# Optimization experiments

Measured on AMD Instinct MI355X. Metric: run time of the kernel, lower is better.

## Reference

```python
import jax, jax.numpy as jnp
import numpy as np
from jax import lax

V, D, L = 32000, 1024, 8
HQ, HKV, HD = 16, 4, 64          # head_dim = D // HQ
H = int(2.6875 * D)              # SwiGLU hidden = 2752
B, S = 2, 1024
WINDOW, GEVERY = 256, 4
EPS, BASE = 1e-6, 10000.0
STD = 0.02


def setup_inputs() -> dict:
    key = jax.random.key(0)
    ks = jax.random.split(key, 10)
    return {
        "idx": jax.random.randint(ks[0], (B, S), 0, V, dtype=jnp.int32),
        "emb": jax.random.normal(ks[1], (V, D), jnp.float32) * STD,
        "Wq": jax.random.normal(ks[2], (L, D, HQ * HD), jnp.float32) * STD,
        "Wk": jax.random.normal(ks[3], (L, D, HKV * HD), jnp.float32) * STD,
        "Wv": jax.random.normal(ks[4], (L, D, HKV * HD), jnp.float32) * STD,
        "Wo": jax.random.normal(ks[5], (L, HQ * HD, D), jnp.float32) * (STD / np.sqrt(2 * L)).astype(np.float32),
        "w1": jax.random.normal(ks[6], (L, D, H), jnp.float32) * STD,
        "w3": jax.random.normal(ks[7], (L, D, H), jnp.float32) * STD,
        "w2": jax.random.normal(ks[8], (L, H, D), jnp.float32) * (STD / np.sqrt(2 * L)).astype(np.float32),
        "n1": jnp.ones((L, D), jnp.float32),
        "n2": jnp.ones((L, D), jnp.float32),
        "nf": jnp.ones((D,), jnp.float32),
    }


def _rmsnorm(x, w):
    return x * lax.rsqrt(jnp.mean(x * x, axis=-1, keepdims=True) + EPS) * w


def _rope(x, cos, sin):
    # x: [B,S,h,HD]; pairs (even, odd) rotated by complex multiply with e^{i*theta}
    x2 = x.reshape(*x.shape[:-1], HD // 2, 2)
    x0, x1 = x2[..., 0], x2[..., 1]
    r0 = x0 * cos - x1 * sin
    r1 = x0 * sin + x1 * cos
    return jnp.stack([r0, r1], axis=-1).reshape(x.shape)


def _forward(idx, emb, Wq, Wk, Wv, Wo, w1, w3, w2, n1, n2, nf):
    # RoPE cache (RoPECache._build_cache)
    inv_freq = 1.0 / (BASE ** (jnp.arange(0, HD, 2, dtype=jnp.float32) / HD))
    t = jnp.arange(S, dtype=jnp.float32)
    freqs = t[:, None] * inv_freq[None, :]                      # [S, HD//2]
    cos = jnp.cos(freqs)[None, :, None, :]                      # [1,S,1,HD//2]
    sin = jnp.sin(freqs)[None, :, None, :]

    # masks: global causal and sliding-window causal (additive, 0 / -inf)
    pos = jnp.arange(S)
    causal = pos[None, :] <= pos[:, None]
    local = causal & ((pos[:, None] - pos[None, :]) < WINDOW)
    neg_inf = jnp.float32(-jnp.inf)
    gmask = jnp.where(causal, 0.0, neg_inf).astype(jnp.float32)
    lmask = jnp.where(local, 0.0, neg_inf).astype(jnp.float32)
    use_global = ((jnp.arange(L) + 1) % GEVERY) == 0            # [L] bool

    scale = 1.0 / (HD ** 0.5)
    rep = HQ // HKV

    def block(x, p):
        wq, wk, wv, wo, W1, W3, W2, g1, g2, ug = p
        h = _rmsnorm(x, g1)
        q = (h @ wq).reshape(B, S, HQ, HD)
        k = (h @ wk).reshape(B, S, HKV, HD)
        v = (h @ wv).reshape(B, S, HKV, HD)
        q = _rope(q, cos, sin)
        k = _rope(k, cos, sin)
        k = jnp.repeat(k, rep, axis=2)                          # GQA: expand KV heads
        v = jnp.repeat(v, rep, axis=2)
        mask = jnp.where(ug, gmask, lmask)
        sc = jnp.einsum('bqhd,bkhd->bhqk', q, k) * scale + mask
        attn = jax.nn.softmax(sc, axis=-1)
        o = jnp.einsum('bhqk,bkhd->bqhd', attn, v).reshape(B, S, HQ * HD)
        x = x + o @ wo
        h2 = _rmsnorm(x, g2)
        x = x + (jax.nn.silu(h2 @ W1) * (h2 @ W3)) @ W2
        return x, None

    x = emb[idx]                                                # token embedding
    x, _ = lax.scan(block, x, (Wq, Wk, Wv, Wo, w1, w3, w2, n1, n2, use_global))
    logits = _rmsnorm(x, nf) @ emb.T                            # tied lm_head
    return logits


def reference(idx, emb, Wq, Wk, Wv, Wo, w1, w3, w2, n1, n2, nf):
    return _forward(idx, emb, Wq, Wk, Wv, Wo, w1, w3, w2, n1, n2, nf)
```

## Files before the change

### kernel.cpp

```cpp
#include <hip/hip_runtime.h>

#define V_ 32000
#define D_ 1024
#define L_ 8
#define HQ_ 16
#define HKV_ 4
#define HD_ 64
#define H_ 2752
#define B_ 2
#define S_ 1024
#define BS_ 2048
#define WINDOW_ 256

typedef float f32x4 __attribute__((ext_vector_type(4)));
typedef short s16x8 __attribute__((ext_vector_type(8)));
typedef unsigned short u16;

__device__ __forceinline__ u16 f2b(float f) {
  union { float f; unsigned u; } a; a.f = f;
  return (u16)((a.u + 0x7fffu + ((a.u >> 16) & 1u)) >> 16);
}
__device__ __forceinline__ float b2f(u16 b) {
  union { unsigned u; float f; } a; a.u = ((unsigned)b) << 16; return a.f;
}

__device__ __forceinline__ void gload_lds16(const void* g, void* l) {
  __builtin_amdgcn_global_load_lds(
      (const __attribute__((address_space(1))) void*)(unsigned long long)(uintptr_t)g,
      (__attribute__((address_space(3))) void*)(unsigned int)(uintptr_t)l,
      16, 0, 0);
}

__global__ void k_cvt(const float* __restrict__ src, u16* __restrict__ dst, long n4) {
  long i = (long)blockIdx.x * blockDim.x + threadIdx.x;
  if (i >= n4) return;
  float4 v = ((const float4*)src)[i];
  ushort4 o; o.x = f2b(v.x); o.y = f2b(v.y); o.z = f2b(v.z); o.w = f2b(v.w);
  ((ushort4*)dst)[i] = o;
}

struct TMat { const float* src; u16* dst; int R, C, t0, mul, add; };
struct T7 { TMat m[7]; };

__global__ void k_transpose7(T7 P) {
  __shared__ float tile[32][33];
  int bid = blockIdx.x;
  int mi = 0;
#pragma unroll
  for (int i = 1; i < 7; ++i) if (bid >= P.m[i].t0) mi = i;
  TMat mm = P.m[mi];
  int tl = bid - mm.t0;
  int ct = mm.C >> 5;
  int tr = tl / ct, tc = tl - tr * ct;
  int r0 = tr << 5, c0 = tc << 5;
  int tx = threadIdx.x & 31, ty = threadIdx.x >> 5;
#pragma unroll
  for (int j = 0; j < 4; ++j)
    tile[ty + j * 8][tx] = mm.src[(size_t)(r0 + ty + j * 8) * mm.C + c0 + tx];
  __syncthreads();
#pragma unroll
  for (int j = 0; j < 4; ++j)
    mm.dst[((size_t)(c0 + ty + j * 8) * mm.mul + mm.add) * mm.R + r0 + tx] =
        f2b(tile[tx][ty + j * 8]);
}

__global__ void k_embed(const int* __restrict__ idx, const float* __restrict__ emb,
                        float* __restrict__ x) {
  int t = blockIdx.x;
  int token = idx[t];
  const float4* s = (const float4*)(emb + (size_t)token * D_);
  float4* d = (float4*)(x + (size_t)t * D_);
  d[threadIdx.x] = s[threadIdx.x];
}

__global__ void k_rmsnorm(const float* __restrict__ x, const float* __restrict__ w,
                          u16* __restrict__ out) {
  int row = blockIdx.x, tid = threadIdx.x;
  float4 v = ((const float4*)(x + (size_t)row * D_))[tid];
  float ss = v.x * v.x + v.y * v.y + v.z * v.z + v.w * v.w;
#pragma unroll
  for (int m = 1; m < 64; m <<= 1) ss += __shfl_xor(ss, m, 64);
  __shared__ float red[4];
  if ((tid & 63) == 0) red[tid >> 6] = ss;
  __syncthreads();
  float tot = red[0] + red[1] + red[2] + red[3];
  float rs = rsqrtf(tot * (1.0f / D_) + 1e-6f);
  float4 wv = ((const float4*)w)[tid];
  ushort4 o;
  o.x = f2b(v.x * rs * wv.x); o.y = f2b(v.y * rs * wv.y);
  o.z = f2b(v.z * rs * wv.z); o.w = f2b(v.w * rs * wv.w);
  ((ushort4*)(out + (size_t)row * D_))[tid] = o;
}

__global__ void k_ropetab(float* __restrict__ cosT, float* __restrict__ sinT) {
  int i = blockIdx.x * blockDim.x + threadIdx.x;
  int s = i >> 5, d = i & 31;
  float inv = __expf(-((float)(2 * d) / (float)HD_) * logf(10000.0f));
  float f = (float)s * inv;
  cosT[i] = cosf(f); sinT[i] = sinf(f);
}

__global__ void k_rope(const float* __restrict__ qkvf, const float* __restrict__ cosT,
                       const float* __restrict__ sinT, u16* __restrict__ qh,
                       u16* __restrict__ kh) {
  int t = blockIdx.x;
  int b = t >> 10, s = t & (S_ - 1);
  int tid = threadIdx.x;
  const float* row = qkvf + (size_t)t * 1536;
  for (int p = tid; p < 512; p += 256) {
    int hh = p >> 5, d = p & 31;
    float x0 = row[hh * 64 + 2 * d], x1 = row[hh * 64 + 2 * d + 1];
    float c = cosT[s * 32 + d], sn = sinT[s * 32 + d];
    size_t o = ((size_t)(b * HQ_ + hh) * S_ + s) * HD_ + 2 * d;
    qh[o] = f2b(x0 * c - x1 * sn);
    qh[o + 1] = f2b(x0 * sn + x1 * c);
  }
  if (tid < 128) {
    int hh = tid >> 5, d = tid & 31;
    float x0 = row[1024 + hh * 64 + 2 * d], x1 = row[1024 + hh * 64 + 2 * d + 1];
    float c = cosT[s * 32 + d], sn = sinT[s * 32 + d];
    size_t o = ((size_t)(b * HKV_ + hh) * S_ + s) * HD_ + 2 * d;
    kh[o] = f2b(x0 * c - x1 * sn);
    kh[o + 1] = f2b(x0 * sn + x1 * c);
  }
}

__global__ void k_vtrans(const float* __restrict__ qkvf, u16* __restrict__ vth) {
  __shared__ float tile[32][65];
  const int s0 = blockIdx.x << 5, hh = blockIdx.y, b = blockIdx.z;
  const int tx = threadIdx.x & 63, ty = threadIdx.x >> 6;
#pragma unroll
  for (int j = 0; j < 8; ++j) {
    int sl = j * 4 + ty;
    tile[sl][tx] = qkvf[(size_t)((b << 10) + s0 + sl) * 1536 + 1280 + hh * 64 + tx];
  }
  __syncthreads();
  const int sx = threadIdx.x & 31, dr = threadIdx.x >> 5;
#pragma unroll
  for (int j = 0; j < 8; ++j) {
    int d = j * 8 + dr;
    vth[((size_t)((b * HKV_ + hh) << 6) + d) * S_ + s0 + sx] = f2b(tile[sx][d]);
  }
}

template <int EPI>
__global__ __launch_bounds__(256) void k_gemm(const u16* __restrict__ A,
                                              const u16* __restrict__ BT,
                                              void* __restrict__ Cp, int kdepth,
                                              int lda, int ldc) {
  __shared__ u16 As[3][4096];
  __shared__ u16 Bs[3][4096];
  const int tid = threadIdx.x;
  const int lane = tid & 63, wid = tid >> 6;
  const int lin = blockIdx.y * 16 + blockIdx.x;
  const int cpx = (gridDim.x * gridDim.y) >> 3;
  const int swz = (lin & 7) * cpx + (lin >> 3);
  const int m0 = (swz & 15) << 7, n0 = (swz >> 4) << 7;
  const int wm = (wid >> 1) << 6, wn = (wid & 1) << 6;
  const int fr = lane & 15, fg = lane >> 4;

  f32x4 acc[4][4] = {};

  const int srow = (wid << 4) + (lane >> 2);
  const int scol = ((lane & 3) - ((lane >> 3) & 3)) & 3;
  const int kz = blockIdx.z * kdepth;
  const u16* ga = A + (size_t)(m0 + srow) * lda + kz + (scol << 3);
  const u16* gb = BT + (size_t)(n0 + srow) * lda + kz + (scol << 3);
  const int cb = wid << 9;

  auto stage = [&](int buf, int k0) {
    u16* la = &As[buf][cb];
    u16* lb = &Bs[buf][cb];
    gload_lds16(ga + k0, la);
    gload_lds16(ga + (size_t)64 * lda + k0, la + 2048);
    gload_lds16(gb + k0, lb);
    gload_lds16(gb + (size_t)64 * lda + k0, lb + 2048);
  };

  const int nk = kdepth >> 5;
  stage(0, 0);
  stage(1, 32);

  const int ab = (wid >> 1) << 2, bb = (wid & 1) << 2;
  const int foff = (fr << 5) + ((((fg + (fr >> 1)) & 3)) << 3);
  int cur = 0;
  for (int t = 0; t < nk; ++t) {
    if (t + 2 < nk) {
      int nb = cur + 2; if (nb >= 3) nb -= 3;
      stage(nb, (t + 2) << 5);
      asm volatile("s_waitcnt vmcnt(8)" ::: "memory");
    } else if (t + 2 == nk) {
      asm volatile("s_waitcnt vmcnt(4)" ::: "memory");
    } else {
      asm volatile("s_waitcnt vmcnt(0)" ::: "memory");
    }
    __builtin_amdgcn_s_barrier();
    s16x8 af[4], bq[4];
#pragma unroll
    for (int i = 0; i < 4; ++i) {
      af[i] = *(const s16x8*)(&As[cur][((ab + i) << 9) + foff]);
      bq[i] = *(const s16x8*)(&Bs[cur][((bb + i) << 9) + foff]);
    }
#pragma unroll
    for (int mi = 0; mi < 4; ++mi)
#pragma unroll
      for (int ni = 0; ni < 4; ++ni)
        acc[mi][ni] = __builtin_amdgcn_mfma_f32_16x16x32_bf16(af[mi], bq[ni], acc[mi][ni], 0, 0, 0);
    __builtin_amdgcn_s_barrier();
    if (++cur == 3) cur = 0;
  }

#pragma unroll
  for (int mi = 0; mi < 4; ++mi) {
#pragma unroll
    for (int ni = 0; ni < 4; ++ni) {
#pragma unroll
      for (int r = 0; r < 4; ++r) {
        int row = m0 + wm + mi * 16 + fg * 4 + r;
        int col = n0 + wn + ni * 16 + fr;
        size_t off = (size_t)row * ldc + col;
        float v = acc[mi][ni][r];
        if (EPI == 0) ((float*)Cp)[off] = v;
        else atomicAdd((float*)Cp + off, v);
      }
    }
  }
}

template <int EPI>
__global__ __launch_bounds__(256, 2) void k_gemm2(const u16* __restrict__ A,
                                                  const u16* __restrict__ BT,
                                                  void* __restrict__ Cp, int K, int ldc) {
  __shared__ u16 As[3][8192];
  __shared__ u16 Bs[3][4096];
  const int tid = threadIdx.x;
  const int lane = tid & 63, wid = tid >> 6;
  const int lin = blockIdx.y * gridDim.x + blockIdx.x;
  const int cpx = (gridDim.x * gridDim.y) >> 3;
  const int swz = (lin & 7) * cpx + (lin >> 3);
  const int m0 = (swz & 7) << 8, n0 = (swz >> 3) << 7;
  const int fr = lane & 15, fg = lane >> 4;

  f32x4 acc[4][8] = {};

  const int srow = lane >> 2;
  const int scol = ((lane & 3) - ((lane >> 3) & 3)) & 3;
  const u16* ga = A + (size_t)(m0 + (wid << 6) + srow) * K + (scol << 3);
  const u16* gb = BT + (size_t)(n0 + (wid << 5) + srow) * K + (scol << 3);
  const int cba = wid << 11;
  const int cbb = wid << 10;

  auto stage = [&](int buf, int k0) {
    u16* la = &As[buf][cba];
    u16* lb = &Bs[buf][cbb];
    gload_lds16(ga + k0, la);
    gload_lds16(ga + (size_t)16 * K + k0, la + 512);
    gload_lds16(ga + (size_t)32 * K + k0, la + 1024);
    gload_lds16(ga + (size_t)48 * K + k0, la + 1536);
    gload_lds16(gb + k0, lb);
    gload_lds16(gb + (size_t)16 * K + k0, lb + 512);
  };

  const int nk = K >> 5;
  stage(0, 0);
  stage(1, 32);

  const int foff = (fr << 5) + ((((fg + (fr >> 1)) & 3)) << 3);
  int cur = 0;
  for (int t = 0; t < nk; ++t) {
    if (t + 2 < nk) {
      int nb = cur + 2; if (nb >= 3) nb -= 3;
      stage(nb, (t + 2) << 5);
      asm volatile("s_waitcnt vmcnt(12)" ::: "memory");
    } else if (t + 2 == nk) {
      asm volatile("s_waitcnt vmcnt(6)" ::: "memory");
    } else {
      asm volatile("s_waitcnt vmcnt(0)" ::: "memory");
    }
    __builtin_amdgcn_s_barrier();
    s16x8 af[4], bq[8];
#pragma unroll
    for (int i = 0; i < 4; ++i)
      af[i] = *(const s16x8*)(&As[cur][(((wid << 2) + i) << 9) + foff]);
#pragma unroll
    for (int j = 0; j < 8; ++j)
      bq[j] = *(const s16x8*)(&Bs[cur][(j << 9) + foff]);
#pragma unroll
    for (int mi = 0; mi < 4; ++mi)
#pragma unroll
      for (int ni = 0; ni < 8; ++ni)
        acc[mi][ni] = __builtin_amdgcn_mfma_f32_16x16x32_bf16(af[mi], bq[ni], acc[mi][ni], 0, 0, 0);
    __builtin_amdgcn_s_barrier();
    if (++cur == 3) cur = 0;
  }

#pragma unroll
  for (int mi = 0; mi < 4; ++mi) {
#pragma unroll
    for (int ni = 0; ni < 8; ++ni) {
#pragma unroll
      for (int r = 0; r < 4; ++r) {
        int row = m0 + (wid << 6) + mi * 16 + fg * 4 + r;
        int col = n0 + ni * 16 + fr;
        float v = acc[mi][ni][r];
        if (EPI == 0) {
          ((float*)Cp)[(size_t)row * ldc + col] = v;
        } else {
          float o = __shfl_xor(v, 1, 64);
          if (!(fr & 1)) {
            float s = v / (1.0f + __expf(-v)) * o;
            ((u16*)Cp)[(size_t)row * ldc + (col >> 1)] = f2b(s);
          }
        }
      }
    }
  }
}

__global__ __launch_bounds__(256) void k_attn(const u16* __restrict__ qh,
                                              const u16* __restrict__ kh,
                                              const u16* __restrict__ vth,
                                              u16* __restrict__ attno, int isGlobal) {
  __shared__ u16 pb[4][512];
  const int qblk = blockIdx.x, hq = blockIdx.y, b = blockIdx.z;
  const int lane = threadIdx.x & 63, wid = threadIdx.x >> 6;
  const int fr = lane & 15, fg = lane >> 4;
  const int q0 = (qblk << 6) + (wid << 4);
  const int hk = hq >> 2;
  const u16* Q = qh + ((size_t)(b * HQ_ + hq) * S_) * HD_;
  const u16* Kh = kh + ((size_t)(b * HKV_ + hk) * S_) * HD_;
  const u16* VT = vth + ((size_t)(b * HKV_ + hk) * HD_) * S_;
  u16* pbuf = pb[wid];

  const s16x8 aq0 = *(const s16x8*)(Q + (q0 + fr) * HD_ + fg * 8);
  const s16x8 aq1 = *(const s16x8*)(Q + (q0 + fr) * HD_ + 32 + fg * 8);

  f32x4 o0 = {}, o1 = {}, o2 = {}, o3 = {};
  float m[4], l[4];
#pragma unroll
  for (int r = 0; r < 4; ++r) { m[r] = -1e30f; l[r] = 0.0f; }

  int kt0 = 0;
  if (!isGlobal) { int lo = q0 - (WINDOW_ - 1); if (lo > 0) kt0 = lo & ~31; }
  const int ktend = q0 + 16;

  for (int kt = kt0; kt < ktend; kt += 32) {
    f32x4 sc0 = {}, sc1 = {};
    {
      s16x8 b0 = *(const s16x8*)(Kh + (kt + fr) * HD_ + fg * 8);
      s16x8 b1 = *(const s16x8*)(Kh + (kt + fr) * HD_ + 32 + fg * 8);
      sc0 = __builtin_amdgcn_mfma_f32_16x16x32_bf16(aq0, b0, sc0, 0, 0, 0);
      sc0 = __builtin_amdgcn_mfma_f32_16x16x32_bf16(aq1, b1, sc0, 0, 0, 0);
      s16x8 c0 = *(const s16x8*)(Kh + (kt + 16 + fr) * HD_ + fg * 8);
      s16x8 c1 = *(const s16x8*)(Kh + (kt + 16 + fr) * HD_ + 32 + fg * 8);
      sc1 = __builtin_amdgcn_mfma_f32_16x16x32_bf16(aq0, c0, sc1, 0, 0, 0);
      sc1 = __builtin_amdgcn_mfma_f32_16x16x32_bf16(aq1, c1, sc1, 0, 0, 0);
    }
#pragma unroll
    for (int r = 0; r < 4; ++r) {
      int row = q0 + fg * 4 + r;
      int col0 = kt + fr, col1 = kt + 16 + fr;
      bool v0 = (col0 <= row) && (isGlobal || (row - col0) < WINDOW_);
      bool v1 = (col1 <= row) && (isGlobal || (row - col1) < WINDOW_);
      float s0 = v0 ? sc0[r] * 0.125f : -1e30f;
      float s1 = v1 ? sc1[r] * 0.125f : -1e30f;
      float t = fmaxf(s0, s1);
#pragma unroll
      for (int msk = 1; msk < 16; msk <<= 1) t = fmaxf(t, __shfl_xor(t, msk, 16));
      float mn = fmaxf(m[r], t);
      float fsc = __expf(m[r] - mn);
      m[r] = mn;
      float p0 = v0 ? __expf(s0 - mn) : 0.0f;
      float p1 = v1 ? __expf(s1 - mn) : 0.0f;
      float ps = p0 + p1;
#pragma unroll
      for (int msk = 1; msk < 16; msk <<= 1) ps += __shfl_xor(ps, msk, 16);
      l[r] = l[r] * fsc + ps;
      o0[r] *= fsc; o1[r] *= fsc; o2[r] *= fsc; o3[r] *= fsc;
      pbuf[(fg * 4 + r) * 32 + fr] = f2b(p0);
      pbuf[(fg * 4 + r) * 32 + 16 + fr] = f2b(p1);
    }
    s16x8 ap = *(const s16x8*)(pbuf + fr * 32 + fg * 8);
    {
      s16x8 bv0 = *(const s16x8*)(VT + (size_t)(0 + fr) * S_ + kt + fg * 8);
      o0 = __builtin_amdgcn_mfma_f32_16x16x32_bf16(ap, bv0, o0, 0, 0, 0);
      s16x8 bv1 = *(const s16x8*)(VT + (size_t)(16 + fr) * S_ + kt + fg * 8);
      o1 = __builtin_amdgcn_mfma_f32_16x16x32_bf16(ap, bv1, o1, 0, 0, 0);
      s16x8 bv2 = *(const s16x8*)(VT + (size_t)(32 + fr) * S_ + kt + fg * 8);
      o2 = __builtin_amdgcn_mfma_f32_16x16x32_bf16(ap, bv2, o2, 0, 0, 0);
      s16x8 bv3 = *(const s16x8*)(VT + (size_t)(48 + fr) * S_ + kt + fg * 8);
      o3 = __builtin_amdgcn_mfma_f32_16x16x32_bf16(ap, bv3, o3, 0, 0, 0);
    }
  }

#pragma unroll
  for (int r = 0; r < 4; ++r) {
    int row = q0 + fg * 4 + r;
    float inv = 1.0f / l[r];
    size_t base = ((size_t)b * S_ + row) * (HQ_ * HD_) + hq * HD_;
    attno[base + fr] = f2b(o0[r] * inv);
    attno[base + 16 + fr] = f2b(o1[r] * inv);
    attno[base + 32 + fr] = f2b(o2[r] * inv);
    attno[base + 48 + fr] = f2b(o3[r] * inv);
  }
}

extern "C" void kernel_launch(void* const* d_in, const int* in_sizes, int n_in,
                              void* d_out, int out_size, void* d_ws, size_t ws_size,
                              hipStream_t stream) {
  (void)in_sizes; (void)n_in; (void)out_size; (void)ws_size;
  const int* idx = (const int*)d_in[0];
  const float* emb = (const float*)d_in[1];
  const float* Wq = (const float*)d_in[2];
  const float* Wk = (const float*)d_in[3];
  const float* Wv = (const float*)d_in[4];
  const float* Wo = (const float*)d_in[5];
  const float* w1 = (const float*)d_in[6];
  const float* w3 = (const float*)d_in[7];
  const float* w2 = (const float*)d_in[8];
  const float* n1 = (const float*)d_in[9];
  const float* n2 = (const float*)d_in[10];
  const float* nf = (const float*)d_in[11];
  float* out = (float*)d_out;

  char* p = (char*)d_ws;
  auto carve = [&](size_t bytes) {
    char* q = p;
    p += (bytes + 255) & ~(size_t)255;
    return (void*)q;
  };
  float* x = (float*)carve((size_t)BS_ * D_ * 4);
  u16* h = (u16*)carve((size_t)BS_ * D_ * 2);
  float* qkvf = (float*)carve((size_t)BS_ * 1536 * 4);
  u16* qh = (u16*)carve((size_t)B_ * HQ_ * S_ * HD_ * 2);
  u16* khb = (u16*)carve((size_t)B_ * HKV_ * S_ * HD_ * 2);
  u16* vth = (u16*)carve((size_t)B_ * HKV_ * HD_ * S_ * 2);
  u16* attno = (u16*)carve((size_t)BS_ * D_ * 2);
  u16* g = (u16*)carve((size_t)BS_ * H_ * 2);
  u16* wT = (u16*)carve((size_t)11075584 * 2);
  float* cosT = (float*)carve((size_t)S_ * 32 * 4);
  float* sinT = (float*)carve((size_t)S_ * 32 * 4);
  u16* embb = (u16*)carve((size_t)V_ * D_ * 2);

  k_cvt<<<V_ * D_ / 4 / 256, 256, 0, stream>>>(emb, embb, (long)V_ * D_ / 4);
  k_ropetab<<<S_ * 32 / 256, 256, 0, stream>>>(cosT, sinT);
  k_embed<<<BS_, 256, 0, stream>>>(idx, emb, x);

  for (int l = 0; l < L_; ++l) {
    T7 t7;
    t7.m[0] = { Wq + (size_t)l * D_ * 1024, wT, D_, 1024, 0, 1, 0 };
    t7.m[1] = { Wk + (size_t)l * D_ * 256, wT + 1048576, D_, 256, 1024, 1, 0 };
    t7.m[2] = { Wv + (size_t)l * D_ * 256, wT + 1310720, D_, 256, 1280, 1, 0 };
    t7.m[3] = { Wo + (size_t)l * 1024 * D_, wT + 1572864, 1024, D_, 1536, 1, 0 };
    t7.m[4] = { w1 + (size_t)l * D_ * H_, wT + 2621440, D_, H_, 2560, 2, 0 };
    t7.m[5] = { w3 + (size_t)l * D_ * H_, wT + 2621440, D_, H_, 5312, 2, 1 };
    t7.m[6] = { w2 + (size_t)l * H_ * D_, wT + 8257536, H_, D_, 8064, 1, 0 };
    k_transpose7<<<10816, 256, 0, stream>>>(t7);

    k_rmsnorm<<<BS_, 256, 0, stream>>>(x, n1 + (size_t)l * D_, h);
    k_gemm<0><<<dim3(16, 12), 256, 0, stream>>>(h, wT, qkvf, 1024, 1024, 1536);
    k_rope<<<BS_, 256, 0, stream>>>(qkvf, cosT, sinT, qh, khb);
    k_vtrans<<<dim3(32, HKV_, B_), 256, 0, stream>>>(qkvf, vth);
    int ig = ((l + 1) % 4) == 0;
    k_attn<<<dim3(16, HQ_, B_), 256, 0, stream>>>(qh, khb, vth, attno, ig);
    k_gemm<4><<<dim3(16, 8, 2), 256, 0, stream>>>(attno, wT + 1572864, x, 512, 1024, 1024);
    k_rmsnorm<<<BS_, 256, 0, stream>>>(x, n2 + (size_t)l * D_, h);
    k_gemm2<3><<<dim3(8, 43), 256, 0, stream>>>(h, wT + 2621440, g, 1024, 2752);
    k_gemm<4><<<dim3(16, 8, 2), 256, 0, stream>>>(g, wT + 8257536, x, 1376, 2752, 1024);
  }

  k_rmsnorm<<<BS_, 256, 0, stream>>>(x, nf, h);
  k_gemm2<0><<<dim3(8, 250), 256, 0, stream>>>(h, embb, out, 1024, 32000);
}
```

Before: 1.520 ms.

## Fuse rope and V transpose kernels; split gemm2 tile across 8 waves

Merges the RoPE kernel and the V-transpose kernel into one launch, using block-index ranges to pick the role, which removes one launch per layer. The 256x128 GEMM used for the SwiGLU up-projection and the LM head now runs with 512 threads (8 waves). Each wave computes a 64x64 sub-tile instead of 64x128, with fewer accumulators and loads per wave, aiming for more latency hiding and lower register pressure. The cost is more barrier participants and less register-level reuse per wave, and the SwiGLU epilogue pairing via shfl_xor still depends on column parity within each wave.

```diff
diff --git a/kernel.cpp b/kernel.cpp
--- a/kernel.cpp
+++ b/kernel.cpp
@@ -100,46 +100,48 @@
   cosT[i] = cosf(f); sinT[i] = sinf(f);
 }
 
-__global__ void k_rope(const float* __restrict__ qkvf, const float* __restrict__ cosT,
-                       const float* __restrict__ sinT, u16* __restrict__ qh,
-                       u16* __restrict__ kh) {
-  int t = blockIdx.x;
-  int b = t >> 10, s = t & (S_ - 1);
+__global__ void k_ropev(const float* __restrict__ qkvf, const float* __restrict__ cosT,
+                        const float* __restrict__ sinT, u16* __restrict__ qh,
+                        u16* __restrict__ kh, u16* __restrict__ vth) {
+  __shared__ float tile[32][65];
+  int bid = blockIdx.x;
   int tid = threadIdx.x;
-  const float* row = qkvf + (size_t)t * 1536;
-  for (int p = tid; p < 512; p += 256) {
-    int hh = p >> 5, d = p & 31;
-    float x0 = row[hh * 64 + 2 * d], x1 = row[hh * 64 + 2 * d + 1];
-    float c = cosT[s * 32 + d], sn = sinT[s * 32 + d];
-    size_t o = ((size_t)(b * HQ_ + hh) * S_ + s) * HD_ + 2 * d;
-    qh[o] = f2b(x0 * c - x1 * sn);
-    qh[o + 1] = f2b(x0 * sn + x1 * c);
-  }
-  if (tid < 128) {
-    int hh = tid >> 5, d = tid & 31;
-    float x0 = row[1024 + hh * 64 + 2 * d], x1 = row[1024 + hh * 64 + 2 * d + 1];
-    float c = cosT[s * 32 + d], sn = sinT[s * 32 + d];
-    size_t o = ((size_t)(b * HKV_ + hh) * S_ + s) * HD_ + 2 * d;
-    kh[o] = f2b(x0 * c - x1 * sn);
-    kh[o + 1] = f2b(x0 * sn + x1 * c);
-  }
-}
-
-__global__ void k_vtrans(const float* __restrict__ qkvf, u16* __restrict__ vth) {
-  __shared__ float tile[32][65];
-  const int s0 = blockIdx.x << 5, hh = blockIdx.y, b = blockIdx.z;
-  const int tx = threadIdx.x & 63, ty = threadIdx.x >> 6;
-#pragma unroll
-  for (int j = 0; j < 8; ++j) {
-    int sl = j * 4 + ty;
-    tile[sl][tx] = qkvf[(size_t)((b << 10) + s0 + sl) * 1536 + 1280 + hh * 64 + tx];
-  }
-  __syncthreads();
-  const int sx = threadIdx.x & 31, dr = threadIdx.x >> 5;
-#pragma unroll
-  for (int j = 0; j < 8; ++j) {
-    int d = j * 8 + dr;
-    vth[((size_t)((b * HKV_ + hh) << 6) + d) * S_ + s0 + sx] = f2b(tile[sx][d]);
+  if (bid < BS_) {
+    int t = bid;
+    int b = t >> 10, s = t & (S_ - 1);
+    const float* row = qkvf + (size_t)t * 1536;
+    for (int p = tid; p < 512; p += 256) {
+      int hh = p >> 5, d = p & 31;
+      float x0 = row[hh * 64 + 2 * d], x1 = row[hh * 64 + 2 * d + 1];
+      float c = cosT[s * 32 + d], sn = sinT[s * 32 + d];
+      size_t o = ((size_t)(b * HQ_ + hh) * S_ + s) * HD_ + 2 * d;
+      qh[o] = f2b(x0 * c - x1 * sn);
+      qh[o + 1] = f2b(x0 * sn + x1 * c);
+    }
+    if (tid < 128) {
+      int hh = tid >> 5, d = tid & 31;
+      float x0 = row[1024 + hh * 64 + 2 * d], x1 = row[1024 + hh * 64 + 2 * d + 1];
+      float c = cosT[s * 32 + d], sn = sinT[s * 32 + d];
+      size_t o = ((size_t)(b * HKV_ + hh) * S_ + s) * HD_ + 2 * d;
+      kh[o] = f2b(x0 * c - x1 * sn);
+      kh[o + 1] = f2b(x0 * sn + x1 * c);
+    }
+  } else {
+    int v = bid - BS_;
+    const int s0 = (v & 31) << 5, hh = (v >> 5) & 3, b = v >> 7;
+    const int tx = tid & 63, ty = tid >> 6;
+#pragma unroll
+    for (int j = 0; j < 8; ++j) {
+      int sl = j * 4 + ty;
+      tile[sl][tx] = qkvf[(size_t)((b << 10) + s0 + sl) * 1536 + 1280 + hh * 64 + tx];
+    }
+    __syncthreads();
+    const int sx = tid & 31, dr = tid >> 5;
+#pragma unroll
+    for (int j = 0; j < 8; ++j) {
+      int d = j * 8 + dr;
+      vth[((size_t)((b * HKV_ + hh) << 6) + d) * S_ + s0 + sx] = f2b(tile[sx][d]);
+    }
   }
 }
 
@@ -228,7 +230,7 @@
 }
 
 template <int EPI>
-__global__ __launch_bounds__(256, 2) void k_gemm2(const u16* __restrict__ A,
+__global__ __launch_bounds__(512, 4) void k_gemm2(const u16* __restrict__ A,
                                                   const u16* __restrict__ BT,
                                                   void* __restrict__ Cp, int K, int ldc) {
   __shared__ u16 As[3][8192];
@@ -241,54 +243,50 @@
   const int m0 = (swz & 7) << 8, n0 = (swz >> 3) << 7;
   const int fr = lane & 15, fg = lane >> 4;
 
-  f32x4 acc[4][8] = {};
+  f32x4 acc[4][4] = {};
 
   const int srow = lane >> 2;
   const int scol = ((lane & 3) - ((lane >> 3) & 3)) & 3;
-  const u16* ga = A + (size_t)(m0 + (wid << 6) + srow) * K + (scol << 3);
-  const u16* gb = BT + (size_t)(n0 + (wid << 5) + srow) * K + (scol << 3);
-  const int cba = wid << 11;
-  const int cbb = wid << 10;
+  const u16* ga = A + (size_t)(m0 + (wid << 5) + srow) * K + (scol << 3);
+  const u16* gb = BT + (size_t)(n0 + (wid << 4) + srow) * K + (scol << 3);
+  const int cba = wid << 10;
+  const int cbb = wid << 9;
 
   auto stage = [&](int buf, int k0) {
-    u16* la = &As[buf][cba];
-    u16* lb = &Bs[buf][cbb];
-    gload_lds16(ga + k0, la);
-    gload_lds16(ga + (size_t)16 * K + k0, la + 512);
-    gload_lds16(ga + (size_t)32 * K + k0, la + 1024);
-    gload_lds16(ga + (size_t)48 * K + k0, la + 1536);
-    gload_lds16(gb + k0, lb);
-    gload_lds16(gb + (size_t)16 * K + k0, lb + 512);
+    gload_lds16(ga + k0, &As[buf][cba]);
+    gload_lds16(ga + (size_t)16 * K + k0, &As[buf][cba + 512]);
+    gload_lds16(gb + k0, &Bs[buf][cbb]);
   };
 
   const int nk = K >> 5;
   stage(0, 0);
   stage(1, 32);
 
+  const int am = (wid >> 1) << 2;
+  const int bn = (wid & 1) << 2;
   const int foff = (fr << 5) + ((((fg + (fr >> 1)) & 3)) << 3);
   int cur = 0;
   for (int t = 0; t < nk; ++t) {
     if (t + 2 < nk) {
       int nb = cur + 2; if (nb >= 3) nb -= 3;
       stage(nb, (t + 2) << 5);
-      asm volatile("s_waitcnt vmcnt(12)" ::: "memory");
+      asm volatile("s_waitcnt vmcnt(6)" ::: "memory");
     } else if (t + 2 == nk) {
-      asm volatile("s_waitcnt vmcnt(6)" ::: "memory");
+      asm volatile("s_waitcnt vmcnt(3)" ::: "memory");
     } else {
       asm volatile("s_waitcnt vmcnt(0)" ::: "memory");
     }
     __builtin_amdgcn_s_barrier();
-    s16x8 af[4], bq[8];
-#pragma unroll
-    for (int i = 0; i < 4; ++i)
-      af[i] = *(const s16x8*)(&As[cur][(((wid << 2) + i) << 9) + foff]);
-#pragma unroll
-    for (int j = 0; j < 8; ++j)
-      bq[j] = *(const s16x8*)(&Bs[cur][(j << 9) + foff]);
+    s16x8 af[4], bq[4];
+#pragma unroll
+    for (int i = 0; i < 4; ++i) {
+      af[i] = *(const s16x8*)(&As[cur][((am + i) << 9) + foff]);
+      bq[i] = *(const s16x8*)(&Bs[cur][((bn + i) << 9) + foff]);
+    }
 #pragma unroll
     for (int mi = 0; mi < 4; ++mi)
 #pragma unroll
-      for (int ni = 0; ni < 8; ++ni)
+      for (int ni = 0; ni < 4; ++ni)
         acc[mi][ni] = __builtin_amdgcn_mfma_f32_16x16x32_bf16(af[mi], bq[ni], acc[mi][ni], 0, 0, 0);
     __builtin_amdgcn_s_barrier();
     if (++cur == 3) cur = 0;
@@ -297,11 +295,11 @@
 #pragma unroll
   for (int mi = 0; mi < 4; ++mi) {
 #pragma unroll
-    for (int ni = 0; ni < 8; ++ni) {
+    for (int ni = 0; ni < 4; ++ni) {
 #pragma unroll
       for (int r = 0; r < 4; ++r) {
-        int row = m0 + (wid << 6) + mi * 16 + fg * 4 + r;
-        int col = n0 + ni * 16 + fr;
+        int row = m0 + ((wid >> 1) << 6) + mi * 16 + fg * 4 + r;
+        int col = n0 + ((wid & 1) << 6) + ni * 16 + fr;
         float v = acc[mi][ni][r];
         if (EPI == 0) {
           ((float*)Cp)[(size_t)row * ldc + col] = v;
@@ -459,16 +457,15 @@
 
     k_rmsnorm<<<BS_, 256, 0, stream>>>(x, n1 + (size_t)l * D_, h);
     k_gemm<0><<<dim3(16, 12), 256, 0, stream>>>(h, wT, qkvf, 1024, 1024, 1536);
-    k_rope<<<BS_, 256, 0, stream>>>(qkvf, cosT, sinT, qh, khb);
-    k_vtrans<<<dim3(32, HKV_, B_), 256, 0, stream>>>(qkvf, vth);
+    k_ropev<<<BS_ + 256, 256, 0, stream>>>(qkvf, cosT, sinT, qh, khb, vth);
     int ig = ((l + 1) % 4) == 0;
     k_attn<<<dim3(16, HQ_, B_), 256, 0, stream>>>(qh, khb, vth, attno, ig);
     k_gemm<4><<<dim3(16, 8, 2), 256, 0, stream>>>(attno, wT + 1572864, x, 512, 1024, 1024);
     k_rmsnorm<<<BS_, 256, 0, stream>>>(x, n2 + (size_t)l * D_, h);
-    k_gemm2<3><<<dim3(8, 43), 256, 0, stream>>>(h, wT + 2621440, g, 1024, 2752);
+    k_gemm2<3><<<dim3(8, 43), 512, 0, stream>>>(h, wT + 2621440, g, 1024, 2752);
     k_gemm<4><<<dim3(16, 8, 2), 256, 0, stream>>>(g, wT + 8257536, x, 1376, 2752, 1024);
   }
 
   k_rmsnorm<<<BS_, 256, 0, stream>>>(x, nf, h);
-  k_gemm2<0><<<dim3(8, 250), 256, 0, stream>>>(h, embb, out, 1024, 32000);
-}
+  k_gemm2<0><<<dim3(8, 250), 512, 0, stream>>>(h, embb, out, 1024, 32000);
+}
```

Result: no change. 1.496 ms (-1.6%).
